# Kernel optimization log

Measured on AMD Instinct MI355X. Metric: run time of the kernel, lower is better.

Reference implementation:

```python
import jax, jax.numpy as jnp
import numpy as np

N_NODES = 100000
N_EDGES = 1600000
IN_DIM = 256
OUT_DIM = 128
BATCH = 8192
SLOPE = 0.1
EPS = 1e-8


def setup_inputs() -> dict:
    key = jax.random.key(0)
    k1, k2, k3, k4, k5, k6, k7 = jax.random.split(key, 7)
    feats = jax.random.normal(k1, (N_NODES, IN_DIM), dtype=jnp.float32)
    W = jax.random.normal(k2, (IN_DIM, OUT_DIM), dtype=jnp.float32) / np.sqrt(IN_DIM)
    b = jax.random.normal(k3, (OUT_DIM,), dtype=jnp.float32) * 0.01
    a = jax.random.normal(k4, (2 * OUT_DIM,), dtype=jnp.float32) / np.sqrt(2 * OUT_DIM)
    r = jax.random.randint(k5, (N_EDGES,), 0, N_NODES, dtype=jnp.int64)
    c = jax.random.randint(k6, (N_EDGES,), 0, N_NODES, dtype=jnp.int64)
    batch_idx = jax.random.randint(k7, (BATCH,), 0, N_NODES, dtype=jnp.int64)
    return {"feats": feats, "W": W, "b": b, "a": a, "r": r, "c": c, "batch_idx": batch_idx}


def reference(feats, W, b, a, r, c, batch_idx):
    d = W.shape[1]
    new_emb = feats @ W + b                      # [N, d]
    # [h_r || h_c] @ a  ==  h_r @ a[:d] + h_c @ a[d:]
    s_src = new_emb @ a[:d]                      # [N]
    s_dst = new_emb @ a[d:]                      # [N]
    e = jnp.exp(jax.nn.leaky_relu(s_src[r] + s_dst[c], negative_slope=SLOPE))  # [E]
    denom = jax.ops.segment_sum(e, r, num_segments=N_NODES)                    # [N]
    num = jax.ops.segment_sum(e[:, None] * new_emb[c], r, num_segments=N_NODES)  # [N, d]
    out = num / (denom[:, None] + EPS)
    return out[batch_idx]
```

## Files before the change

### kernel.cpp

```cpp
#include <hip/hip_runtime.h>

#define N_NODES 100000
#define N_EDGES 1600000
#define IN_DIM  256
#define OUT_DIM 128
#define BATCH_N 8192
#define SLOPE   0.1f
#define EPS_V   1e-8f
#define BUCKET_CAP 96

__global__ __launch_bounds__(256) void prep_kernel(const float* __restrict__ W,
                                                   const float* __restrict__ b,
                                                   const float* __restrict__ a,
                                                   float* __restrict__ uv,
                                                   float* __restrict__ consts) {
  int t = threadIdx.x;
  float su = 0.f, sv = 0.f;
  for (int j = 0; j < OUT_DIM; j++) {
    float w = W[t * OUT_DIM + j];
    su += w * a[j];
    sv += w * a[OUT_DIM + j];
  }
  uv[t] = su;
  uv[IN_DIM + t] = sv;

  __shared__ float red[256];
  float pb = (t < OUT_DIM) ? b[t] : 0.f;
  red[t] = (t < OUT_DIM) ? pb * a[t] : 0.f;
  __syncthreads();
  for (int off = 128; off > 0; off >>= 1) {
    if (t < off) red[t] += red[t + off];
    __syncthreads();
  }
  if (t == 0) consts[0] = red[0];
  __syncthreads();
  red[t] = (t < OUT_DIM) ? pb * a[OUT_DIM + t] : 0.f;
  __syncthreads();
  for (int off = 128; off > 0; off >>= 1) {
    if (t < off) red[t] += red[t + off];
    __syncthreads();
  }
  if (t == 0) consts[1] = red[0];
}

__global__ __launch_bounds__(256) void init_kernel(int* __restrict__ slot, int* __restrict__ cursor) {
  int i = blockIdx.x * blockDim.x + threadIdx.x;
  if (i < N_NODES) slot[i] = -1;
  if (i < BATCH_N) cursor[i] = 0;
}

__global__ __launch_bounds__(256) void slots_kernel(const int* __restrict__ batch_idx, int* __restrict__ slot) {
  int i = blockIdx.x * blockDim.x + threadIdx.x;
  if (i < BATCH_N) slot[batch_idx[i]] = i;
}

__global__ __launch_bounds__(256) void scores_kernel(const float* __restrict__ feats,
                                                     const float* __restrict__ uv,
                                                     const float* __restrict__ consts,
                                                     float* __restrict__ s_src,
                                                     float* __restrict__ s_dst) {
  int wid = (blockIdx.x * blockDim.x + threadIdx.x) >> 6;
  int lane = threadIdx.x & 63;
  if (wid >= N_NODES) return;
  float4 f  = *(const float4*)&feats[(size_t)wid * IN_DIM + lane * 4];
  float4 u4 = *(const float4*)&uv[lane * 4];
  float4 v4 = *(const float4*)&uv[IN_DIM + lane * 4];
  float p1 = f.x * u4.x + f.y * u4.y + f.z * u4.z + f.w * u4.w;
  float p2 = f.x * v4.x + f.y * v4.y + f.z * v4.z + f.w * v4.w;
#pragma unroll
  for (int s = 32; s > 0; s >>= 1) {
    p1 += __shfl_xor(p1, s);
    p2 += __shfl_xor(p2, s);
  }
  if (lane == 0) {
    s_src[wid] = p1 + consts[0];
    s_dst[wid] = p2 + consts[1];
  }
}

__global__ __launch_bounds__(256) void scatter_kernel(const int* __restrict__ r, const int* __restrict__ c,
                                                      const int* __restrict__ slot,
                                                      const float* __restrict__ s_src,
                                                      const float* __restrict__ s_dst,
                                                      int* __restrict__ cursor,
                                                      int* __restrict__ bucket_c, float* __restrict__ bucket_e) {
  int i = blockIdx.x * blockDim.x + threadIdx.x;
  if (i >= N_EDGES) return;
  int rr = r[i];
  int sl = slot[rr];
  if (sl < 0) return;
  int cc = c[i];
  float x = s_src[rr] + s_dst[cc];
  float lr = x > 0.f ? x : SLOPE * x;
  float e = expf(lr);
  int pos = atomicAdd(&cursor[sl], 1);
  if (pos < BUCKET_CAP) {
    bucket_c[sl * BUCKET_CAP + pos] = cc;
    bucket_e[sl * BUCKET_CAP + pos] = e;
  }
}

__global__ __launch_bounds__(256) void agg_kernel(const float* __restrict__ feats,
                                                  const int* __restrict__ cursor,
                                                  const int* __restrict__ bucket_c,
                                                  const float* __restrict__ bucket_e,
                                                  float* __restrict__ aggw,
                                                  float* __restrict__ scale_b) {
  __shared__ int   sc[BUCKET_CAP];
  __shared__ float se[BUCKET_CAP];
  __shared__ float red[4][256];
  __shared__ float dred[4];
  const int sl = blockIdx.x;
  const int t = threadIdx.x, w = t >> 6, lane = t & 63;
  int cnt = cursor[sl];
  cnt = cnt > BUCKET_CAP ? BUCKET_CAP : cnt;
  if (t < cnt) {
    sc[t] = bucket_c[sl * BUCKET_CAP + t];
    se[t] = bucket_e[sl * BUCKET_CAP + t];
  }
  __syncthreads();
  float ax = 0.f, ay = 0.f, az = 0.f, aw = 0.f, den = 0.f;
#pragma unroll 2
  for (int j = w; j < cnt; j += 4) {
    int cc  = sc[j];
    float e = se[j];
    float4 f = *(const float4*)&feats[(size_t)cc * IN_DIM + lane * 4];
    ax += e * f.x; ay += e * f.y; az += e * f.z; aw += e * f.w;
    den += e;
  }
  *(float4*)&red[w][lane * 4] = make_float4(ax, ay, az, aw);
  if (lane == 0) dred[w] = den;
  __syncthreads();
  if (w == 0) {
    float4 r0 = *(float4*)&red[0][lane * 4];
    float4 r1 = *(float4*)&red[1][lane * 4];
    float4 r2 = *(float4*)&red[2][lane * 4];
    float4 r3 = *(float4*)&red[3][lane * 4];
    float d = dred[0] + dred[1] + dred[2] + dred[3];
    float dinv = 1.f / (d + EPS_V);
    *(float4*)&aggw[(size_t)sl * IN_DIM + lane * 4] =
        make_float4((r0.x + r1.x + r2.x + r3.x) * dinv,
                    (r0.y + r1.y + r2.y + r3.y) * dinv,
                    (r0.z + r1.z + r2.z + r3.z) * dinv,
                    (r0.w + r1.w + r2.w + r3.w) * dinv);
    if (lane == 0) scale_b[sl] = d * dinv;
  }
}

__global__ __launch_bounds__(256) void gemm2_kernel(const float* __restrict__ aggw,
                                                    const float* __restrict__ W,
                                                    const float* __restrict__ b,
                                                    const float* __restrict__ scale_b,
                                                    float* __restrict__ out) {
  __shared__ float As[32][33];
  __shared__ float Ws[32][128];
  const int t = threadIdx.x;
  const int row0 = blockIdx.x * 32;
  const int tx = t & 31;
  const int ty = t >> 5;

  float acc[4][4];
#pragma unroll
  for (int i = 0; i < 4; i++)
#pragma unroll
    for (int j = 0; j < 4; j++) acc[i][j] = 0.f;

  for (int k0 = 0; k0 < IN_DIM; k0 += 32) {
    {
      int row = t >> 3, c4 = t & 7;
      float4 v = *(const float4*)&aggw[(size_t)(row0 + row) * IN_DIM + k0 + c4 * 4];
      As[c4 * 4 + 0][row] = v.x;
      As[c4 * 4 + 1][row] = v.y;
      As[c4 * 4 + 2][row] = v.z;
      As[c4 * 4 + 3][row] = v.w;
    }
#pragma unroll
    for (int p = 0; p < 4; p++) {
      int id = t + p * 256;
      int kr = id >> 5, c4 = id & 31;
      *(float4*)&Ws[kr][c4 * 4] = *(const float4*)&W[(size_t)(k0 + kr) * OUT_DIM + c4 * 4];
    }
    __syncthreads();
#pragma unroll
    for (int k = 0; k < 32; k++) {
      float av[4];
#pragma unroll
      for (int i = 0; i < 4; i++) av[i] = As[k][ty * 4 + i];
      float4 w4 = *(const float4*)&Ws[k][tx * 4];
#pragma unroll
      for (int i = 0; i < 4; i++) {
        acc[i][0] += av[i] * w4.x; acc[i][1] += av[i] * w4.y;
        acc[i][2] += av[i] * w4.z; acc[i][3] += av[i] * w4.w;
      }
    }
    __syncthreads();
  }
  float4 b4 = *(const float4*)&b[tx * 4];
#pragma unroll
  for (int i = 0; i < 4; i++) {
    int row = row0 + ty * 4 + i;
    float sb = scale_b[row];
    *(float4*)&out[(size_t)row * OUT_DIM + tx * 4] =
        make_float4(acc[i][0] + sb * b4.x, acc[i][1] + sb * b4.y,
                    acc[i][2] + sb * b4.z, acc[i][3] + sb * b4.w);
  }
}

__global__ __launch_bounds__(256) void fix_kernel(const int* __restrict__ batch_idx,
                                                  const int* __restrict__ slot,
                                                  float* __restrict__ out) {
  int wid = (blockIdx.x * blockDim.x + threadIdx.x) >> 6;
  int lane = threadIdx.x & 63;
  if (wid >= BATCH_N) return;
  int sl = slot[batch_idx[wid]];
  if (sl == wid) return;
  float2 v = *(const float2*)&out[(size_t)sl * OUT_DIM + lane * 2];
  *(float2*)&out[(size_t)wid * OUT_DIM + lane * 2] = v;
}

extern "C" void kernel_launch(void* const* d_in, const int* in_sizes, int n_in,
                              void* d_out, int out_size, void* d_ws, size_t ws_size,
                              hipStream_t stream) {
  const float* feats     = (const float*)d_in[0];
  const float* W         = (const float*)d_in[1];
  const float* b         = (const float*)d_in[2];
  const float* a         = (const float*)d_in[3];
  const int*   r         = (const int*)d_in[4];
  const int*   c         = (const int*)d_in[5];
  const int*   batch_idx = (const int*)d_in[6];
  float* out = (float*)d_out;

  float* uv       = (float*)d_ws;
  float* consts   = uv + 2 * IN_DIM;
  float* s_src    = consts + 8;
  float* s_dst    = s_src + N_NODES;
  int*   slot     = (int*)(s_dst + N_NODES);
  int*   cursor   = slot + N_NODES;
  float* scale_b  = (float*)(cursor + BATCH_N);
  int*   bucket_c = (int*)(scale_b + BATCH_N);
  float* bucket_e = (float*)(bucket_c + (size_t)BATCH_N * BUCKET_CAP);
  float* aggw     = bucket_e + (size_t)BATCH_N * BUCKET_CAP;

  prep_kernel<<<1, 256, 0, stream>>>(W, b, a, uv, consts);
  init_kernel<<<(N_NODES + 255) / 256, 256, 0, stream>>>(slot, cursor);
  slots_kernel<<<(BATCH_N + 255) / 256, 256, 0, stream>>>(batch_idx, slot);
  scores_kernel<<<(N_NODES * 64 + 255) / 256, 256, 0, stream>>>(feats, uv, consts, s_src, s_dst);
  scatter_kernel<<<(N_EDGES + 255) / 256, 256, 0, stream>>>(r, c, slot, s_src, s_dst,
                                                            cursor, bucket_c, bucket_e);
  agg_kernel<<<BATCH_N, 256, 0, stream>>>(feats, cursor, bucket_c, bucket_e, aggw, scale_b);
  gemm2_kernel<<<BATCH_N / 32, 256, 0, stream>>>(aggw, W, b, scale_b, out);
  fix_kernel<<<(BATCH_N * 64 + 255) / 256, 256, 0, stream>>>(batch_idx, slot, out);
}
```

Baseline: 245.1 us.

## Drop slot-array init, merge setup kernels, fold duplicate fixup into GEMM

Merges the prep, init and slots kernels into one setup launch and stops resetting the 100k-entry slot array. Stale slot values are instead checked in the scatter kernel by confirming batch_idx[slot] matches the row. The final fix kernel is removed: the GEMM now reads aggw rows through slot[batch_idx[row]], so duplicate batch entries resolve during the GEMM. This saves two launches and a memset-like pass, at the cost of an extra dependent gather in scatter and indirect row loads in the GEMM.

New measurement: 228.3 us. 1.07x faster.

```diff
diff --git a/kernel.cpp b/kernel.cpp
--- a/kernel.cpp
+++ b/kernel.cpp
@@ -9,12 +9,21 @@
 #define EPS_V   1e-8f
 #define BUCKET_CAP 96
 
-__global__ __launch_bounds__(256) void prep_kernel(const float* __restrict__ W,
-                                                   const float* __restrict__ b,
-                                                   const float* __restrict__ a,
-                                                   float* __restrict__ uv,
-                                                   float* __restrict__ consts) {
-  int t = threadIdx.x;
+__global__ __launch_bounds__(256) void setup_kernel(const float* __restrict__ W,
+                                                    const float* __restrict__ b,
+                                                    const float* __restrict__ a,
+                                                    const int* __restrict__ batch_idx,
+                                                    int* __restrict__ slot,
+                                                    int* __restrict__ cursor,
+                                                    float* __restrict__ uv,
+                                                    float* __restrict__ consts) {
+  const int blk = blockIdx.x, t = threadIdx.x;
+  if (blk < 32) {
+    int i = blk * 256 + t;
+    slot[batch_idx[i]] = i;
+    cursor[i] = 0;
+    return;
+  }
   float su = 0.f, sv = 0.f;
   for (int j = 0; j < OUT_DIM; j++) {
     float w = W[t * OUT_DIM + j];
@@ -41,17 +50,6 @@
     __syncthreads();
   }
   if (t == 0) consts[1] = red[0];
-}
-
-__global__ __launch_bounds__(256) void init_kernel(int* __restrict__ slot, int* __restrict__ cursor) {
-  int i = blockIdx.x * blockDim.x + threadIdx.x;
-  if (i < N_NODES) slot[i] = -1;
-  if (i < BATCH_N) cursor[i] = 0;
-}
-
-__global__ __launch_bounds__(256) void slots_kernel(const int* __restrict__ batch_idx, int* __restrict__ slot) {
-  int i = blockIdx.x * blockDim.x + threadIdx.x;
-  if (i < BATCH_N) slot[batch_idx[i]] = i;
 }
 
 __global__ __launch_bounds__(256) void scores_kernel(const float* __restrict__ feats,
@@ -80,6 +78,7 @@
 
 __global__ __launch_bounds__(256) void scatter_kernel(const int* __restrict__ r, const int* __restrict__ c,
                                                       const int* __restrict__ slot,
+                                                      const int* __restrict__ batch_idx,
                                                       const float* __restrict__ s_src,
                                                       const float* __restrict__ s_dst,
                                                       int* __restrict__ cursor,
@@ -88,7 +87,8 @@
   if (i >= N_EDGES) return;
   int rr = r[i];
   int sl = slot[rr];
-  if (sl < 0) return;
+  if (sl < 0 || sl >= BATCH_N) return;
+  if (batch_idx[sl] != rr) return;
   int cc = c[i];
   float x = s_src[rr] + s_dst[cc];
   float lr = x > 0.f ? x : SLOPE * x;
@@ -151,14 +151,20 @@
                                                     const float* __restrict__ W,
                                                     const float* __restrict__ b,
                                                     const float* __restrict__ scale_b,
+                                                    const int* __restrict__ batch_idx,
+                                                    const int* __restrict__ slot,
                                                     float* __restrict__ out) {
   __shared__ float As[32][33];
   __shared__ float Ws[32][128];
+  __shared__ int ridx[32];
   const int t = threadIdx.x;
   const int row0 = blockIdx.x * 32;
   const int tx = t & 31;
   const int ty = t >> 5;
 
+  if (t < 32) ridx[t] = slot[batch_idx[row0 + t]];
+  __syncthreads();
+
   float acc[4][4];
 #pragma unroll
   for (int i = 0; i < 4; i++)
@@ -168,7 +174,7 @@
   for (int k0 = 0; k0 < IN_DIM; k0 += 32) {
     {
       int row = t >> 3, c4 = t & 7;
-      float4 v = *(const float4*)&aggw[(size_t)(row0 + row) * IN_DIM + k0 + c4 * 4];
+      float4 v = *(const float4*)&aggw[(size_t)ridx[row] * IN_DIM + k0 + c4 * 4];
       As[c4 * 4 + 0][row] = v.x;
       As[c4 * 4 + 1][row] = v.y;
       As[c4 * 4 + 2][row] = v.z;
@@ -199,23 +205,11 @@
 #pragma unroll
   for (int i = 0; i < 4; i++) {
     int row = row0 + ty * 4 + i;
-    float sb = scale_b[row];
+    float sb = scale_b[ridx[ty * 4 + i]];
     *(float4*)&out[(size_t)row * OUT_DIM + tx * 4] =
         make_float4(acc[i][0] + sb * b4.x, acc[i][1] + sb * b4.y,
                     acc[i][2] + sb * b4.z, acc[i][3] + sb * b4.w);
   }
-}
-
-__global__ __launch_bounds__(256) void fix_kernel(const int* __restrict__ batch_idx,
-                                                  const int* __restrict__ slot,
-                                                  float* __restrict__ out) {
-  int wid = (blockIdx.x * blockDim.x + threadIdx.x) >> 6;
-  int lane = threadIdx.x & 63;
-  if (wid >= BATCH_N) return;
-  int sl = slot[batch_idx[wid]];
-  if (sl == wid) return;
-  float2 v = *(const float2*)&out[(size_t)sl * OUT_DIM + lane * 2];
-  *(float2*)&out[(size_t)wid * OUT_DIM + lane * 2] = v;
 }
 
 extern "C" void kernel_launch(void* const* d_in, const int* in_sizes, int n_in,
@@ -241,13 +235,10 @@
   float* bucket_e = (float*)(bucket_c + (size_t)BATCH_N * BUCKET_CAP);
   float* aggw     = bucket_e + (size_t)BATCH_N * BUCKET_CAP;
 
-  prep_kernel<<<1, 256, 0, stream>>>(W, b, a, uv, consts);
-  init_kernel<<<(N_NODES + 255) / 256, 256, 0, stream>>>(slot, cursor);
-  slots_kernel<<<(BATCH_N + 255) / 256, 256, 0, stream>>>(batch_idx, slot);
+  setup_kernel<<<33, 256, 0, stream>>>(W, b, a, batch_idx, slot, cursor, uv, consts);
   scores_kernel<<<(N_NODES * 64 + 255) / 256, 256, 0, stream>>>(feats, uv, consts, s_src, s_dst);
-  scatter_kernel<<<(N_EDGES + 255) / 256, 256, 0, stream>>>(r, c, slot, s_src, s_dst,
+  scatter_kernel<<<(N_EDGES + 255) / 256, 256, 0, stream>>>(r, c, slot, batch_idx, s_src, s_dst,
                                                             cursor, bucket_c, bucket_e);
   agg_kernel<<<BATCH_N, 256, 0, stream>>>(feats, cursor, bucket_c, bucket_e, aggw, scale_b);
-  gemm2_kernel<<<BATCH_N / 32, 256, 0, stream>>>(aggw, W, b, scale_b, out);
-  fix_kernel<<<(BATCH_N * 64 + 255) / 256, 256, 0, stream>>>(batch_idx, slot, out);
-}
+  gemm2_kernel<<<BATCH_N / 32, 256, 0, stream>>>(aggw, W, b, scale_b, batch_idx, slot, out);
+}
```
